# Performance work log

Hardware: AMD Instinct MI355X
Metric: run time of the kernel (lower is better)

The kernel has to match this reference:

```python
import jax, jax.numpy as jnp
import numpy as np

BETA = 0.2

def setup_inputs() -> dict:
    key = jax.random.key(0)
    k1, k2 = jax.random.split(key)
    z = jax.random.normal(k1, (32, 256, 32, 32), dtype=jnp.float32)
    # codebook initialized uniform(-1/K, 1/K) as in the torch module
    K, D = 8192, 256
    codebook = jax.random.uniform(k2, (K, D), dtype=jnp.float32, minval=-1.0 / K, maxval=1.0 / K)
    return {"z": z, "codebook": codebook}

def reference(z, codebook):
    b, d, h, w = z.shape
    # (b d h w) -> (b*h*w, d)
    zf = jnp.transpose(z, (0, 2, 3, 1)).reshape(-1, d)
    # squared L2 distances to codebook entries: [N, K]
    dist = (
        jnp.sum(zf * zf, axis=1, keepdims=True)
        + jnp.sum(codebook * codebook, axis=1)
        - 2.0 * jnp.matmul(zf, codebook.T)
    )
    indices = jnp.argmin(dist, axis=1)  # [N]
    # gather == one-hot matmul in value (and in gradient wrt codebook)
    quantized = jnp.take(codebook, indices, axis=0)  # [N, d]
    codebook_loss = jnp.mean((jax.lax.stop_gradient(zf) - quantized) ** 2)
    commitment_loss = BETA * jnp.mean((zf - jax.lax.stop_gradient(quantized)) ** 2)
    # straight-through estimator
    q_st = zf + jax.lax.stop_gradient(quantized - zf)
    q_st = jnp.transpose(q_st.reshape(b, h, w, d), (0, 3, 1, 2))
    return (q_st, codebook_loss, commitment_loss)
```

## Files before the change

kernel.cpp:

```cpp
#include <hip/hip_runtime.h>
#include <hip/hip_bf16.h>
#include <stdint.h>

typedef __attribute__((ext_vector_type(4))) float floatx4;
typedef __attribute__((ext_vector_type(16))) float floatx16;
typedef __attribute__((ext_vector_type(4))) int intx4;
typedef __attribute__((ext_vector_type(8))) int intx8;
typedef __attribute__((ext_vector_type(2))) unsigned int uint2v;
typedef unsigned long long u64;

static constexpr int NROWS = 32768;
static constexpr int NCODE = 8192;
static constexpr int QELEMS = 8388608;
static constexpr float CSCALE = 8192.0f;

__global__ __launch_bounds__(256) void prep_all(
    const float* __restrict__ z, const float* __restrict__ cb,
    unsigned char* __restrict__ z8, unsigned char* __restrict__ c8,
    float* __restrict__ norms, u64* __restrict__ amin)
{
  const int bid = blockIdx.x;
  const int t = threadIdx.x;
  if (bid < 1024) {
    __shared__ float tile[32][260];
    const int b = bid & 31, db = (bid >> 5) & 7, hwb = bid >> 8;
    const int d0 = db * 32, hw0 = hwb * 256;
    const float* src = z + (((size_t)b * 256 + d0) << 10) + hw0;
#pragma unroll
    for (int i = 0; i < 8; ++i) {
      int idx = i * 256 + t;
      int r = idx >> 6, c4 = (idx & 63) * 4;
      *(floatx4*)&tile[r][c4] = *(const floatx4*)&src[((size_t)r << 10) + c4];
    }
    __syncthreads();
    const int dq = t & 3;
    const int hb = t >> 2;
#pragma unroll
    for (int it = 0; it < 4; ++it) {
      int h = hb + it * 64;
      float f[8];
#pragma unroll
      for (int i = 0; i < 8; ++i) f[i] = tile[dq * 8 + i][h];
      int lo = __builtin_amdgcn_cvt_pk_fp8_f32(f[0], f[1], 0, false);
      lo = __builtin_amdgcn_cvt_pk_fp8_f32(f[2], f[3], lo, true);
      int hi = __builtin_amdgcn_cvt_pk_fp8_f32(f[4], f[5], 0, false);
      hi = __builtin_amdgcn_cvt_pk_fp8_f32(f[6], f[7], hi, true);
      uint2v o; o[0] = (unsigned)lo; o[1] = (unsigned)hi;
      *(uint2v*)&z8[((size_t)(b * 1024 + hw0 + h)) * 256 + d0 + dq * 8] = o;
    }
  } else if (bid < 3072) {
    const int k = (bid - 1024) * 4 + (t >> 6);
    const int lane = t & 63;
    floatx4 v = *(const floatx4*)&cb[((size_t)k << 8) + lane * 4];
    float a = v[0] * CSCALE, b2 = v[1] * CSCALE, c = v[2] * CSCALE, d2 = v[3] * CSCALE;
    int r = __builtin_amdgcn_cvt_pk_fp8_f32(a, b2, 0, false);
    r = __builtin_amdgcn_cvt_pk_fp8_f32(c, d2, r, true);
    *(unsigned int*)&c8[((size_t)k << 8) + lane * 4] = (unsigned)r;
    float s = a * a + b2 * b2 + c * c + d2 * d2;
#pragma unroll
    for (int off = 32; off; off >>= 1) s += __shfl_down(s, off);
    if (lane == 0) norms[k] = s;
  } else {
    const int base = (bid - 3072) * 2048;
#pragma unroll
    for (int i = 0; i < 8; ++i) amin[base + i * 256 + t] = ~0ull;
  }
}

__global__ __launch_bounds__(256, 2) void gemm_argmin(
    const unsigned char* __restrict__ z8, const unsigned char* __restrict__ c8,
    const float* __restrict__ norms, u64* __restrict__ amin)
{
  __shared__ alignas(16) unsigned char lds8[69632 + 4096];

  const int tid = threadIdx.x;
  const int lane = tid & 63;
  const int wid = tid >> 6;
  const int wm = wid >> 1;
  const int wn = wid & 1;

  const int bid = blockIdx.x;
  const int swz = (bid & 7) * 1024 + (bid >> 3);
  const int cx = swz & 63;
  const int cy = swz >> 6;
  const int m0 = cx * 128;
  const int n0 = cy * 256;

  const int l31 = lane & 31;
  const int hi = lane >> 5;
  const int k2 = hi << 1;

  intx8 af[2][4];
#pragma unroll
  for (int ti = 0; ti < 2; ++ti) {
    const unsigned char* arow =
        c8 + ((size_t)(m0 + wm * 64 + ti * 32 + l31) << 8) + k2 * 16;
#pragma unroll
    for (int kt = 0; kt < 4; ++kt) {
      intx4 lo = *(const intx4*)(arow + kt * 64);
      intx4 hv = *(const intx4*)(arow + kt * 64 + 16);
      intx8 o;
#pragma unroll
      for (int w = 0; w < 4; ++w) { o[w] = lo[w]; o[4 + w] = hv[w]; }
      af[ti][kt] = o;
    }
  }

  {
    const unsigned char* gsrc = z8 + ((size_t)n0 << 8) + tid * 16;
    unsigned char* dstb = lds8 + (tid >> 4) * 272 + (tid & 15) * 16;
    intx4 tmp[8];
#pragma unroll
    for (int c = 0; c < 8; ++c) tmp[c] = *(const intx4*)(gsrc + c * 4096);
#pragma unroll
    for (int c = 0; c < 8; ++c) *(intx4*)(dstb + c * 4352) = tmp[c];
#pragma unroll
    for (int c = 0; c < 8; ++c) tmp[c] = *(const intx4*)(gsrc + (8 + c) * 4096);
#pragma unroll
    for (int c = 0; c < 8; ++c) *(intx4*)(dstb + (8 + c) * 4352) = tmp[c];
  }
  __syncthreads();

  floatx16 acc[2][4];
#pragma unroll
  for (int i = 0; i < 2; ++i)
#pragma unroll
    for (int j = 0; j < 4; ++j)
#pragma unroll
      for (int e = 0; e < 16; ++e) acc[i][j][e] = 0.f;

  {
    const unsigned char* rb = lds8 + (size_t)(wn * 128 + l31) * 272 + k2 * 16;
#pragma unroll
    for (int kt = 0; kt < 4; ++kt) {
      intx8 bf[4];
#pragma unroll
      for (int tj = 0; tj < 4; ++tj) {
        intx4 lo = *(const intx4*)(rb + tj * 8704 + kt * 64);
        intx4 hv = *(const intx4*)(rb + tj * 8704 + kt * 64 + 16);
        intx8 o;
#pragma unroll
        for (int w = 0; w < 4; ++w) { o[w] = lo[w]; o[4 + w] = hv[w]; }
        bf[tj] = o;
      }
#pragma unroll
      for (int ti = 0; ti < 2; ++ti)
#pragma unroll
        for (int tj = 0; tj < 4; ++tj)
          acc[ti][tj] = __builtin_amdgcn_mfma_scale_f32_32x32x64_f8f6f4(
              af[ti][kt], bf[tj], acc[ti][tj], 0, 0, 0, 127, 0, 127);
    }
  }

  floatx4 nv[2][4];
#pragma unroll
  for (int ti = 0; ti < 2; ++ti)
#pragma unroll
    for (int rq = 0; rq < 4; ++rq)
      nv[ti][rq] = *(const floatx4*)&norms[m0 + wm * 64 + ti * 32 + rq * 8 + 4 * hi];

  u64* best2 = (u64*)(lds8 + 69632);
#pragma unroll
  for (int tj = 0; tj < 4; ++tj) {
    float best = __builtin_inff();
    int bc = 0;
#pragma unroll
    for (int ti = 0; ti < 2; ++ti)
#pragma unroll
      for (int rq = 0; rq < 4; ++rq)
#pragma unroll
        for (int rl = 0; rl < 4; ++rl) {
          float sc = fmaf(acc[ti][tj][rq * 4 + rl], -16384.f, nv[ti][rq][rl]);
          int cd = m0 + wm * 64 + ti * 32 + rq * 8 + 4 * hi + rl;
          if (sc < best) { best = sc; bc = cd; }
        }
    uint32_t u = __float_as_uint(best);
    u ^= ((uint32_t)((int32_t)u >> 31) | 0x80000000u);
    u64 p = ((u64)u << 32) | (uint32_t)bc;
    {
      u64 o = (u64)__shfl_xor((long long)p, 32);
      p = o < p ? o : p;
    }
    if (lane < 32) best2[(size_t)(wn * 128 + tj * 32 + l31) * 2 + wm] = p;
  }
  __syncthreads();
  {
    u64 a = best2[tid * 2], b = best2[tid * 2 + 1];
    u64 p = a < b ? a : b;
    atomicMin(&amin[n0 + tid], p);
  }
}

__global__ __launch_bounds__(256) void gather_out(
    const float* __restrict__ z, const float* __restrict__ cb,
    const u64* __restrict__ amin,
    float* __restrict__ out, float* __restrict__ partial)
{
  const int t = threadIdx.x;
  const size_t e0 = ((size_t)blockIdx.x * 256 + t) * 8;
  const int d = (int)((e0 >> 10) & 255);
  const int b = (int)(e0 >> 18);
  const int n0 = b * 1024 + (int)(e0 & 1023);
  uint32_t kv[8];
#pragma unroll
  for (int m = 0; m < 8; ++m) kv[m] = (uint32_t)amin[n0 + m];
  floatx4 z0 = *(const floatx4*)&z[e0];
  floatx4 z1 = *(const floatx4*)&z[e0 + 4];
  floatx4 q0, q1;
#pragma unroll
  for (int m = 0; m < 4; ++m) {
    q0[m] = cb[((size_t)kv[m] << 8) + d];
    q1[m] = cb[((size_t)kv[4 + m] << 8) + d];
  }
  *(floatx4*)&out[e0] = q0;
  *(floatx4*)&out[e0 + 4] = q1;
  float s = 0.f;
#pragma unroll
  for (int m = 0; m < 4; ++m) {
    float d0 = z0[m] - q0[m], d1 = z1[m] - q1[m];
    s += d0 * d0 + d1 * d1;
  }
#pragma unroll
  for (int off = 32; off; off >>= 1) s += __shfl_down(s, off);
  __shared__ float ps[4];
  if ((t & 63) == 0) ps[t >> 6] = s;
  __syncthreads();
  if (t == 0) partial[blockIdx.x] = ps[0] + ps[1] + ps[2] + ps[3];
}

__global__ __launch_bounds__(256) void finalize(const float* __restrict__ partial,
                                                float* __restrict__ out)
{
  const int t = threadIdx.x;
  float s = 0.f;
#pragma unroll
  for (int i = 0; i < 16; ++i) s += partial[i * 256 + t];
#pragma unroll
  for (int off = 32; off; off >>= 1) s += __shfl_down(s, off);
  __shared__ float ps[4];
  if ((t & 63) == 0) ps[t >> 6] = s;
  __syncthreads();
  if (t == 0) {
    float m = (ps[0] + ps[1] + ps[2] + ps[3]) / (float)QELEMS;
    out[QELEMS] = m;
    out[QELEMS + 1] = 0.2f * m;
  }
}

extern "C" void kernel_launch(void* const* d_in, const int* in_sizes, int n_in,
                              void* d_out, int out_size, void* d_ws, size_t ws_size,
                              hipStream_t stream)
{
  const float* z = (const float*)d_in[0];
  const float* cb = (const float*)d_in[1];
  float* out = (float*)d_out;
  char* ws = (char*)d_ws;

  unsigned char* z8 = (unsigned char*)(ws + 0);
  unsigned char* c8 = (unsigned char*)(ws + 8388608);
  float* norms = (float*)(ws + 10485760);
  u64* amin = (u64*)(ws + 10616832);
  float* lpart = (float*)(ws + 10878976);

  prep_all<<<3088, 256, 0, stream>>>(z, cb, z8, c8, norms, amin);
  gemm_argmin<<<8192, 256, 0, stream>>>(z8, c8, norms, amin);
  gather_out<<<QELEMS / 2048, 256, 0, stream>>>(z, cb, amin, out, lpart);
  finalize<<<1, 256, 0, stream>>>(lpart, out);
}
```

Before: 187.0 us.

## Loop over four row tiles per block and replace atomics with partial-min reduction

Each gemm block now keeps its codebook A fragments and norms in registers and processes four consecutive 256-row z tiles in a loop, instead of one tile per block. This cuts the grid from 8192 to 2048 blocks. The global atomicMin on the packed argmin array is replaced by plain stores into a per-column-block partial buffer, reduced by a new reduce_amin kernel, which also removes the amin init in prep. The cost is an extra kernel launch and about 16 MB of partial-buffer traffic, and the per-tile loads are still not overlapped with compute.

Measured after the change: 156.2 us. -16.4%, faster.

```diff
diff --git a/kernel.cpp b/kernel.cpp
--- a/kernel.cpp
+++ b/kernel.cpp
@@ -6,6 +6,7 @@
 typedef __attribute__((ext_vector_type(16))) float floatx16;
 typedef __attribute__((ext_vector_type(4))) int intx4;
 typedef __attribute__((ext_vector_type(8))) int intx8;
+typedef __attribute__((ext_vector_type(4))) unsigned int uint4v;
 typedef __attribute__((ext_vector_type(2))) unsigned int uint2v;
 typedef unsigned long long u64;
 
@@ -17,7 +18,7 @@
 __global__ __launch_bounds__(256) void prep_all(
     const float* __restrict__ z, const float* __restrict__ cb,
     unsigned char* __restrict__ z8, unsigned char* __restrict__ c8,
-    float* __restrict__ norms, u64* __restrict__ amin)
+    float* __restrict__ norms)
 {
   const int bid = blockIdx.x;
   const int t = threadIdx.x;
@@ -48,7 +49,7 @@
       uint2v o; o[0] = (unsigned)lo; o[1] = (unsigned)hi;
       *(uint2v*)&z8[((size_t)(b * 1024 + hw0 + h)) * 256 + d0 + dq * 8] = o;
     }
-  } else if (bid < 3072) {
+  } else {
     const int k = (bid - 1024) * 4 + (t >> 6);
     const int lane = t & 63;
     floatx4 v = *(const floatx4*)&cb[((size_t)k << 8) + lane * 4];
@@ -60,16 +61,12 @@
 #pragma unroll
     for (int off = 32; off; off >>= 1) s += __shfl_down(s, off);
     if (lane == 0) norms[k] = s;
-  } else {
-    const int base = (bid - 3072) * 2048;
-#pragma unroll
-    for (int i = 0; i < 8; ++i) amin[base + i * 256 + t] = ~0ull;
   }
 }
 
 __global__ __launch_bounds__(256, 2) void gemm_argmin(
     const unsigned char* __restrict__ z8, const unsigned char* __restrict__ c8,
-    const float* __restrict__ norms, u64* __restrict__ amin)
+    const float* __restrict__ norms, u64* __restrict__ partial)
 {
   __shared__ alignas(16) unsigned char lds8[69632 + 4096];
 
@@ -80,11 +77,10 @@
   const int wn = wid & 1;
 
   const int bid = blockIdx.x;
-  const int swz = (bid & 7) * 1024 + (bid >> 3);
+  const int swz = (bid & 7) * 256 + (bid >> 3);
   const int cx = swz & 63;
-  const int cy = swz >> 6;
+  const int cyg = swz >> 6;
   const int m0 = cx * 128;
-  const int n0 = cy * 256;
 
   const int l31 = lane & 31;
   const int hi = lane >> 5;
@@ -106,31 +102,42 @@
     }
   }
 
-  {
-    const unsigned char* gsrc = z8 + ((size_t)n0 << 8) + tid * 16;
-    unsigned char* dstb = lds8 + (tid >> 4) * 272 + (tid & 15) * 16;
-    intx4 tmp[8];
-#pragma unroll
-    for (int c = 0; c < 8; ++c) tmp[c] = *(const intx4*)(gsrc + c * 4096);
-#pragma unroll
-    for (int c = 0; c < 8; ++c) *(intx4*)(dstb + c * 4352) = tmp[c];
-#pragma unroll
-    for (int c = 0; c < 8; ++c) tmp[c] = *(const intx4*)(gsrc + (8 + c) * 4096);
-#pragma unroll
-    for (int c = 0; c < 8; ++c) *(intx4*)(dstb + (8 + c) * 4352) = tmp[c];
-  }
-  __syncthreads();
-
-  floatx16 acc[2][4];
-#pragma unroll
-  for (int i = 0; i < 2; ++i)
-#pragma unroll
-    for (int j = 0; j < 4; ++j)
-#pragma unroll
-      for (int e = 0; e < 16; ++e) acc[i][j][e] = 0.f;
-
-  {
-    const unsigned char* rb = lds8 + (size_t)(wn * 128 + l31) * 272 + k2 * 16;
+  floatx4 nv[2][4];
+#pragma unroll
+  for (int ti = 0; ti < 2; ++ti)
+#pragma unroll
+    for (int rq = 0; rq < 4; ++rq)
+      nv[ti][rq] = *(const floatx4*)&norms[m0 + wm * 64 + ti * 32 + rq * 8 + 4 * hi];
+
+  u64* best2 = (u64*)(lds8 + 69632);
+  const unsigned char* gB0 = z8 + ((size_t)(cyg * 1024) << 8);
+  unsigned char* dstb = lds8 + (tid >> 4) * 272 + (tid & 15) * 16;
+  const unsigned char* rb = lds8 + (size_t)(wn * 128 + l31) * 272 + k2 * 16;
+
+#pragma unroll 1
+  for (int t = 0; t < 4; ++t) {
+    {
+      const unsigned char* gsrc = gB0 + ((size_t)(t * 256) << 8) + tid * 16;
+      intx4 tmp[8];
+#pragma unroll
+      for (int c = 0; c < 8; ++c) tmp[c] = *(const intx4*)(gsrc + c * 4096);
+#pragma unroll
+      for (int c = 0; c < 8; ++c) *(intx4*)(dstb + c * 4352) = tmp[c];
+#pragma unroll
+      for (int c = 0; c < 8; ++c) tmp[c] = *(const intx4*)(gsrc + (8 + c) * 4096);
+#pragma unroll
+      for (int c = 0; c < 8; ++c) *(intx4*)(dstb + (8 + c) * 4352) = tmp[c];
+    }
+    __syncthreads();
+
+    floatx16 acc[2][4];
+#pragma unroll
+    for (int i = 0; i < 2; ++i)
+#pragma unroll
+      for (int j = 0; j < 4; ++j)
+#pragma unroll
+        for (int e = 0; e < 16; ++e) acc[i][j][e] = 0.f;
+
 #pragma unroll
     for (int kt = 0; kt < 4; ++kt) {
       intx8 bf[4];
@@ -150,50 +157,54 @@
           acc[ti][tj] = __builtin_amdgcn_mfma_scale_f32_32x32x64_f8f6f4(
               af[ti][kt], bf[tj], acc[ti][tj], 0, 0, 0, 127, 0, 127);
     }
-  }
-
-  floatx4 nv[2][4];
-#pragma unroll
-  for (int ti = 0; ti < 2; ++ti)
-#pragma unroll
-    for (int rq = 0; rq < 4; ++rq)
-      nv[ti][rq] = *(const floatx4*)&norms[m0 + wm * 64 + ti * 32 + rq * 8 + 4 * hi];
-
-  u64* best2 = (u64*)(lds8 + 69632);
-#pragma unroll
-  for (int tj = 0; tj < 4; ++tj) {
-    float best = __builtin_inff();
-    int bc = 0;
-#pragma unroll
-    for (int ti = 0; ti < 2; ++ti)
-#pragma unroll
-      for (int rq = 0; rq < 4; ++rq)
-#pragma unroll
-        for (int rl = 0; rl < 4; ++rl) {
-          float sc = fmaf(acc[ti][tj][rq * 4 + rl], -16384.f, nv[ti][rq][rl]);
-          int cd = m0 + wm * 64 + ti * 32 + rq * 8 + 4 * hi + rl;
-          if (sc < best) { best = sc; bc = cd; }
-        }
-    uint32_t u = __float_as_uint(best);
-    u ^= ((uint32_t)((int32_t)u >> 31) | 0x80000000u);
-    u64 p = ((u64)u << 32) | (uint32_t)bc;
+
+#pragma unroll
+    for (int tj = 0; tj < 4; ++tj) {
+      float best = __builtin_inff();
+      int bc = 0;
+#pragma unroll
+      for (int ti = 0; ti < 2; ++ti)
+#pragma unroll
+        for (int rq = 0; rq < 4; ++rq)
+#pragma unroll
+          for (int rl = 0; rl < 4; ++rl) {
+            float sc = fmaf(acc[ti][tj][rq * 4 + rl], -16384.f, nv[ti][rq][rl]);
+            int cd = m0 + wm * 64 + ti * 32 + rq * 8 + 4 * hi + rl;
+            if (sc < best) { best = sc; bc = cd; }
+          }
+      uint32_t u = __float_as_uint(best);
+      u ^= ((uint32_t)((int32_t)u >> 31) | 0x80000000u);
+      u64 p = ((u64)u << 32) | (uint32_t)bc;
+      {
+        u64 o = (u64)__shfl_xor((long long)p, 32);
+        p = o < p ? o : p;
+      }
+      if (lane < 32) best2[(size_t)(wn * 128 + tj * 32 + l31) * 2 + wm] = p;
+    }
+    __syncthreads();
     {
-      u64 o = (u64)__shfl_xor((long long)p, 32);
-      p = o < p ? o : p;
-    }
-    if (lane < 32) best2[(size_t)(wn * 128 + tj * 32 + l31) * 2 + wm] = p;
-  }
-  __syncthreads();
-  {
-    u64 a = best2[tid * 2], b = best2[tid * 2 + 1];
-    u64 p = a < b ? a : b;
-    atomicMin(&amin[n0 + tid], p);
-  }
+      u64 a = best2[tid * 2], b = best2[tid * 2 + 1];
+      partial[(size_t)cx * NROWS + cyg * 1024 + t * 256 + tid] = a < b ? a : b;
+    }
+  }
+}
+
+__global__ __launch_bounds__(256) void reduce_amin(const u64* __restrict__ partial,
+                                                   uint32_t* __restrict__ codei)
+{
+  const int n = blockIdx.x * 256 + threadIdx.x;
+  u64 m = partial[n];
+#pragma unroll 8
+  for (int x = 1; x < 64; ++x) {
+    u64 v = partial[(size_t)x * NROWS + n];
+    m = v < m ? v : m;
+  }
+  codei[n] = (uint32_t)m;
 }
 
 __global__ __launch_bounds__(256) void gather_out(
     const float* __restrict__ z, const float* __restrict__ cb,
-    const u64* __restrict__ amin,
+    const uint32_t* __restrict__ codei,
     float* __restrict__ out, float* __restrict__ partial)
 {
   const int t = threadIdx.x;
@@ -201,16 +212,15 @@
   const int d = (int)((e0 >> 10) & 255);
   const int b = (int)(e0 >> 18);
   const int n0 = b * 1024 + (int)(e0 & 1023);
-  uint32_t kv[8];
-#pragma unroll
-  for (int m = 0; m < 8; ++m) kv[m] = (uint32_t)amin[n0 + m];
+  uint4v k0 = *(const uint4v*)&codei[n0];
+  uint4v k1 = *(const uint4v*)&codei[n0 + 4];
   floatx4 z0 = *(const floatx4*)&z[e0];
   floatx4 z1 = *(const floatx4*)&z[e0 + 4];
   floatx4 q0, q1;
 #pragma unroll
   for (int m = 0; m < 4; ++m) {
-    q0[m] = cb[((size_t)kv[m] << 8) + d];
-    q1[m] = cb[((size_t)kv[4 + m] << 8) + d];
+    q0[m] = cb[((size_t)k0[m] << 8) + d];
+    q1[m] = cb[((size_t)k1[m] << 8) + d];
   }
   *(floatx4*)&out[e0] = q0;
   *(floatx4*)&out[e0 + 4] = q1;
@@ -259,11 +269,13 @@
   unsigned char* z8 = (unsigned char*)(ws + 0);
   unsigned char* c8 = (unsigned char*)(ws + 8388608);
   float* norms = (float*)(ws + 10485760);
-  u64* amin = (u64*)(ws + 10616832);
-  float* lpart = (float*)(ws + 10878976);
-
-  prep_all<<<3088, 256, 0, stream>>>(z, cb, z8, c8, norms, amin);
-  gemm_argmin<<<8192, 256, 0, stream>>>(z8, c8, norms, amin);
-  gather_out<<<QELEMS / 2048, 256, 0, stream>>>(z, cb, amin, out, lpart);
+  u64* pamin = (u64*)(ws + 10616832);
+  uint32_t* codei = (uint32_t*)(ws + 27394048);
+  float* lpart = (float*)(ws + 27525120);
+
+  prep_all<<<3072, 256, 0, stream>>>(z, cb, z8, c8, norms);
+  gemm_argmin<<<2048, 256, 0, stream>>>(z8, c8, norms, pamin);
+  reduce_amin<<<NROWS / 256, 256, 0, stream>>>(pamin, codei);
+  gather_out<<<QELEMS / 2048, 256, 0, stream>>>(z, cb, codei, out, lpart);
   finalize<<<1, 256, 0, stream>>>(lpart, out);
 }
```
